# Kernel optimization log

Hardware: AMD Instinct MI355X
Metric: run time of the kernel (lower is better)

Reference implementation:

```python
import jax, jax.numpy as jnp
import numpy as np

B, T, I, H, O = 128, 1024, 512, 1024, 512
LN_EPS = 1e-5

def _linear_params(key, out_dim, in_dim):
    k1, k2 = jax.random.split(key)
    bound = 1.0 / np.sqrt(in_dim)
    W = jax.random.uniform(k1, (out_dim, in_dim), jnp.float32, -bound, bound)
    b = jax.random.uniform(k2, (out_dim,), jnp.float32, -bound, bound)
    return W, b

def setup_inputs() -> dict:
    key = jax.random.key(0)
    ks = jax.random.split(key, 10)
    x = jax.random.normal(ks[0], (B, T, I), jnp.float32)
    Wir, bir = _linear_params(ks[1], H, I)
    Whr, bhr = _linear_params(ks[2], H, H)
    Wiz, biz = _linear_params(ks[3], H, I)
    Whz, bhz = _linear_params(ks[4], H, H)
    Win, bin_ = _linear_params(ks[5], H, I)
    Whn, bhn = _linear_params(ks[6], H, H)
    Wskip, bskip = _linear_params(ks[7], H, I)
    gamma = jnp.ones((H,), jnp.float32)
    beta = jnp.zeros((H,), jnp.float32)
    Wout, bout = _linear_params(ks[8], O, H)
    return dict(x=x, Wir=Wir, bir=bir, Whr=Whr, bhr=bhr, Wiz=Wiz, biz=biz,
                Whz=Whz, bhz=bhz, Win=Win, bin_=bin_, Whn=Whn, bhn=bhn,
                Wskip=Wskip, bskip=bskip, gamma=gamma, beta=beta,
                Wout=Wout, bout=bout)

def reference(x, Wir, bir, Whr, bhr, Wiz, biz, Whz, bhz, Win, bin_, Whn, bhn,
              Wskip, bskip, gamma, beta, Wout, bout):
    # Precompute input-side projections in one batched GEMM each (same math as per-step Linear).
    rx = jnp.einsum('bti,hi->bth', x, Wir) + bir  # (B,T,H)
    zx = jnp.einsum('bti,hi->bth', x, Wiz) + biz
    nx = jnp.einsum('bti,hi->bth', x, Win) + bin_

    def step(h, inp):
        rx_t, zx_t, nx_t = inp
        r = jax.nn.sigmoid(rx_t + h @ Whr.T + bhr)
        z = jax.nn.sigmoid(zx_t + h @ Whz.T + bhz)
        n = jnp.tanh(nx_t + r * (h @ Whn.T + bhn))
        h_new = (1.0 - z) * n + z * h
        return h_new, h_new

    h0 = jnp.zeros((x.shape[0], Whr.shape[0]), x.dtype)
    xs = (jnp.swapaxes(rx, 0, 1), jnp.swapaxes(zx, 0, 1), jnp.swapaxes(nx, 0, 1))
    _, hs = jax.lax.scan(step, h0, xs)  # hs: (T,B,H)
    hs = jnp.swapaxes(hs, 0, 1)  # (B,T,H)

    skip = jnp.einsum('bti,hi->bth', x, Wskip) + bskip
    combined = hs + skip
    mu = jnp.mean(combined, axis=-1, keepdims=True)
    var = jnp.var(combined, axis=-1, keepdims=True)
    normed = (combined - mu) * jax.lax.rsqrt(var + LN_EPS) * gamma + beta
    out = jnp.einsum('bth,oh->bto', normed, Wout) + bout  # (B,T,O)
    return out
```

## Files before the change

### kernel.cpp

```cpp
#include <hip/hip_runtime.h>

#define T_DIM 1024
#define B_DIM 128
#define I_DIM 512
#define H_DIM 1024
#define O_DIM 512
#define TC 64
#define NCHUNK (T_DIM / TC)

typedef _Float16 half8 __attribute__((ext_vector_type(8)));
typedef _Float16 half4v __attribute__((ext_vector_type(4)));
typedef float floatx4 __attribute__((ext_vector_type(4)));
typedef unsigned int uint4v __attribute__((ext_vector_type(4)));

__device__ __forceinline__ void gload_lds16(const void* g, void* l) {
  __builtin_amdgcn_global_load_lds(
      (const __attribute__((address_space(1))) void*)g,
      (__attribute__((address_space(3))) void*)l, 16, 0, 0);
}

__device__ __forceinline__ float sigmoidf_(float x) {
  return 1.f / (1.f + __expf(-x));
}
__device__ __forceinline__ float tanhf_(float x) {
  float e = __expf(fminf(-2.f * x, 60.f));
  return (1.f - e) / (1.f + e);
}

__global__ __launch_bounds__(256) void k_cvt(const float* __restrict__ s,
                                             _Float16* __restrict__ d, int n4) {
  int i = blockIdx.x * 256 + threadIdx.x;
  if (i < n4) {
    float4 v = ((const float4*)s)[i];
    half4v h = {(_Float16)v.x, (_Float16)v.y, (_Float16)v.z, (_Float16)v.w};
    ((half4v*)d)[i] = h;
  }
}

__global__ __launch_bounds__(256) void k_cvt_x(const float* __restrict__ x,
                                               _Float16* __restrict__ x16, int t0) {
  int i = blockIdx.x * 256 + threadIdx.x;
  int i4 = i & 127;
  int row = i >> 7;
  int b = row & 127, tl = row >> 7;
  float4 v = ((const float4*)(x + ((size_t)b * T_DIM + t0 + tl) * I_DIM))[i4];
  half4v h = {(_Float16)v.x, (_Float16)v.y, (_Float16)v.z, (_Float16)v.w};
  ((half4v*)(x16 + (size_t)row * I_DIM))[i4] = h;
}

__global__ __launch_bounds__(256) void build_bcat(const float* __restrict__ a,
                                                  const float* __restrict__ b,
                                                  const float* __restrict__ c,
                                                  const float* __restrict__ d,
                                                  float* __restrict__ o) {
  int i = blockIdx.x * 256 + threadIdx.x;
  if (i < 4096) {
    const float* p = (i < 1024) ? a : (i < 2048) ? b : (i < 3072) ? c : d;
    o[i] = p[i & 1023];
  }
}

template <int MODE>
__global__ __launch_bounds__(256) void gemm_f16(
    const _Float16* __restrict__ A, const _Float16* __restrict__ B,
    const float* __restrict__ bias, _Float16* __restrict__ C16,
    float* __restrict__ C32, int M, int N, int K, int t0) {
  __shared__ __align__(16) _Float16 As[128 * 64];
  __shared__ __align__(16) _Float16 Bs[128 * 64];
  const int tid = threadIdx.x, lane = tid & 63, wv = tid >> 6;
  const int wm = wv >> 1, wn = wv & 1;
  const int lj = lane & 15, lk = lane >> 4;
  const size_t rowA0 = (size_t)blockIdx.y * 128, colB0 = (size_t)blockIdx.x * 128;
  floatx4 acc[4][4] = {};
  for (int kb = 0; kb < K; kb += 64) {
    __syncthreads();
#pragma unroll
    for (int i = 0; i < 4; ++i) {
      int q = i * 256 + tid;
      int r = q >> 3, c = q & 7;
      gload_lds16(A + (rowA0 + r) * (size_t)K + kb + c * 8, As + (size_t)(i * 4 + wv) * 512);
    }
#pragma unroll
    for (int i = 0; i < 4; ++i) {
      int q = i * 256 + tid;
      int r = q >> 3, c = q & 7;
      gload_lds16(B + (colB0 + r) * (size_t)K + kb + c * 8, Bs + (size_t)(i * 4 + wv) * 512);
    }
    __syncthreads();
#pragma unroll
    for (int ks = 0; ks < 2; ++ks) {
      half8 af[4], bf[4];
#pragma unroll
      for (int am = 0; am < 4; ++am)
        af[am] = *(const half8*)(As + (wm * 64 + am * 16 + lj) * 64 + ks * 32 + lk * 8);
#pragma unroll
      for (int bn = 0; bn < 4; ++bn)
        bf[bn] = *(const half8*)(Bs + (wn * 64 + bn * 16 + lj) * 64 + ks * 32 + lk * 8);
#pragma unroll
      for (int am = 0; am < 4; ++am)
#pragma unroll
        for (int bn = 0; bn < 4; ++bn)
          acc[am][bn] = __builtin_amdgcn_mfma_f32_16x16x32_f16(af[am], bf[bn], acc[am][bn], 0, 0, 0);
    }
  }
#pragma unroll
  for (int am = 0; am < 4; ++am)
#pragma unroll
    for (int bn = 0; bn < 4; ++bn)
#pragma unroll
      for (int rr = 0; rr < 4; ++rr) {
        size_t grow = rowA0 + wm * 64 + am * 16 + lk * 4 + rr;
        size_t gcol = colB0 + wn * 64 + bn * 16 + lj;
        float v = acc[am][bn][rr] + bias[gcol];
        if constexpr (MODE == 0) {
          C16[grow * (size_t)N + gcol] = (_Float16)v;
        } else {
          size_t tl = grow >> 7, b = grow & 127;
          C32[b * (size_t)(T_DIM * O_DIM) + (t0 + tl) * (size_t)O_DIM + gcol] = v;
        }
      }
}

__global__ __launch_bounds__(384) void scan_kernel(
    const _Float16* __restrict__ rznx,
    const _Float16* __restrict__ Whcat,
    const float* __restrict__ bhr, const float* __restrict__ bhz,
    const float* __restrict__ bhn,
    _Float16* __restrict__ h16,
    float* __restrict__ h32,
    _Float16* __restrict__ hs16,
    int* __restrict__ flags,
    int chunk) {
  __shared__ __align__(16) _Float16 hlds[16 * 1024];
  __shared__ float exch[2][2][16 * 17];
  __shared__ __align__(16) _Float16 hout[16][32];
  const int tid = threadIdx.x, lane = tid & 63, wv = tid >> 6;
  const int g = wv % 3, jh = wv / 3;
  const int bg = blockIdx.x & 7, js = blockIdx.x >> 3;
  const int b0 = bg * 16;
  const int jbase = js * 32 + jh * 16;
  const int lj = lane & 15, lk = lane >> 4;
  const int jcol = jbase + lj;

  half8 wf[32];
  {
    const _Float16* wb = Whcat + ((size_t)g * 1024 + jcol) * 1024 + lk * 8;
#pragma unroll
    for (int ks = 0; ks < 32; ++ks) wf[ks] = *(const half8*)(wb + ks * 32);
  }
  const float* bh = (g == 0) ? bhr : (g == 1) ? bhz : bhn;
  const float biasg = bh[jcol];
  float hown[4];
  if (g == 1) {
#pragma unroll
    for (int r = 0; r < 4; ++r) hown[r] = h32[(size_t)(b0 + lk * 4 + r) * 1024 + jcol];
  }
  int cur = 0;
  for (int t = 0; t < TC; ++t) {
    const int gs = chunk * TC + t;
    const _Float16* xg = rznx + ((size_t)t * 128 + b0) * 4096 + g * 1024 + jcol;
    float xv[4];
#pragma unroll
    for (int r = 0; r < 4; ++r) xv[r] = (float)xg[(size_t)(lk * 4 + r) * 4096];
    float nxv[4];
    if (g == 1) {
#pragma unroll
      for (int r = 0; r < 4; ++r)
        nxv[r] = (float)rznx[((size_t)t * 128 + b0 + lk * 4 + r) * 4096 + 2048 + jcol];
    }
    if (tid < 256) {
      const _Float16* hsrc = h16 + (size_t)cur * (128 * 1024) + (size_t)b0 * 1024;
      uint4v vv[8];
      const char* ap[8];
#pragma unroll
      for (int i = 0; i < 8; ++i) {
        int q = tid + i * 256;
        int b = q >> 7, c = q & 127;
        ap[i] = (const char*)(hsrc + b * 1024 + c * 8);
      }
#pragma unroll
      for (int i = 0; i < 8; ++i)
        asm volatile("global_load_dwordx4 %0, %1, off sc0 sc1"
                     : "=v"(vv[i]) : "v"(ap[i]));
      asm volatile("s_waitcnt vmcnt(0)" ::: "memory");
#pragma unroll
      for (int i = 0; i < 8; ++i) {
        int q = tid + i * 256;
        int b = q >> 7, c = q & 127;
        *(uint4v*)((char*)hlds + b * 2048 + ((c ^ (b & 7)) * 16)) = vv[i];
      }
    }
    __syncthreads();
    floatx4 acc = {0.f, 0.f, 0.f, 0.f};
#pragma unroll
    for (int ks = 0; ks < 32; ++ks) {
      int c = ks * 4 + lk;
      int b = lj;
      half8 af = *(const half8*)((const char*)hlds + b * 2048 + ((c ^ (b & 7)) * 16));
      acc = __builtin_amdgcn_mfma_f32_16x16x32_f16(af, wf[ks], acc, 0, 0, 0);
    }
    float zv[4] = {0.f, 0.f, 0.f, 0.f};
    if (g == 0) {
#pragma unroll
      for (int r = 0; r < 4; ++r)
        exch[jh][0][(lk * 4 + r) * 17 + lj] = sigmoidf_(acc[r] + biasg + xv[r]);
    } else if (g == 2) {
#pragma unroll
      for (int r = 0; r < 4; ++r)
        exch[jh][1][(lk * 4 + r) * 17 + lj] = acc[r] + biasg;
    } else {
#pragma unroll
      for (int r = 0; r < 4; ++r) zv[r] = sigmoidf_(acc[r] + biasg + xv[r]);
    }
    __syncthreads();
    if (g == 1) {
#pragma unroll
      for (int r = 0; r < 4; ++r) {
        float rr = exch[jh][0][(lk * 4 + r) * 17 + lj];
        float np = exch[jh][1][(lk * 4 + r) * 17 + lj];
        float n = tanhf_(nxv[r] + rr * np);
        float hn = (1.f - zv[r]) * n + zv[r] * hown[r];
        hown[r] = hn;
        hout[lk * 4 + r][jh * 16 + lj] = (_Float16)hn;
      }
    }
    __syncthreads();
    if (wv == 0) {
      int row = lane >> 2, c = lane & 3;
      uint4v hv = *(const uint4v*)((const char*)hout + row * 64 + c * 16);
      char* p1 = (char*)(h16 + (size_t)(cur ^ 1) * (128 * 1024) +
                         (size_t)(b0 + row) * 1024 + js * 32 + c * 8);
      asm volatile("global_store_dwordx4 %0, %1, off sc0 sc1"
                   :: "v"(p1), "v"(hv) : "memory");
      _Float16* p2 = hs16 + ((size_t)t * 128 + b0 + row) * 1024 + js * 32 + c * 8;
      *(uint4v*)p2 = hv;
      asm volatile("s_waitcnt vmcnt(0)" ::: "memory");
      if (lane == 0) {
        int* fp = flags + ((size_t)bg * 32 + js) * 32;
        int val = gs + 1;
        asm volatile("global_store_dword %0, %1, off sc0 sc1"
                     :: "v"(fp), "v"(val) : "memory");
      }
    } else if (wv == 5) {
      const int* fp = flags + ((size_t)bg * 32 + (lane & 31)) * 32;
      const int target = gs + 1;
      int spin = 0;
      while (true) {
        int v;
        asm volatile("global_load_dword %0, %1, off sc0 sc1\n\ts_waitcnt vmcnt(0)"
                     : "=v"(v) : "v"(fp) : "memory");
        if (__all(v >= target)) break;
        __builtin_amdgcn_s_sleep(1);
        if (++spin > (1 << 17)) break;
      }
    }
    __syncthreads();
    cur ^= 1;
  }
  if (g == 1) {
#pragma unroll
    for (int r = 0; r < 4; ++r) h32[(size_t)(b0 + lk * 4 + r) * 1024 + jcol] = hown[r];
  }
}

__global__ __launch_bounds__(256) void ln_kernel(
    const _Float16* __restrict__ hs, const _Float16* __restrict__ rz,
    const float* __restrict__ gamma, const float* __restrict__ beta,
    _Float16* __restrict__ outp) {
  const int row = blockIdx.x, tid = threadIdx.x;
  const int lane = tid & 63, wv = tid >> 6;
  half4v hv = *(const half4v*)(hs + (size_t)row * 1024 + tid * 4);
  half4v sv = *(const half4v*)(rz + (size_t)row * 4096 + 3072 + tid * 4);
  float v[4];
  float s = 0.f, s2 = 0.f;
#pragma unroll
  for (int j = 0; j < 4; ++j) {
    v[j] = (float)hv[j] + (float)sv[j];
    s += v[j];
    s2 += v[j] * v[j];
  }
#pragma unroll
  for (int o = 32; o > 0; o >>= 1) {
    s += __shfl_xor(s, o, 64);
    s2 += __shfl_xor(s2, o, 64);
  }
  __shared__ float ps[4][2];
  if (lane == 0) { ps[wv][0] = s; ps[wv][1] = s2; }
  __syncthreads();
  s = ps[0][0] + ps[1][0] + ps[2][0] + ps[3][0];
  s2 = ps[0][1] + ps[1][1] + ps[2][1] + ps[3][1];
  const float mu = s * (1.f / 1024.f);
  const float var = s2 * (1.f / 1024.f) - mu * mu;
  const float rstd = rsqrtf(var + 1e-5f);
  half4v ov;
#pragma unroll
  for (int j = 0; j < 4; ++j)
    ov[j] = (_Float16)((v[j] - mu) * rstd * gamma[tid * 4 + j] + beta[tid * 4 + j]);
  *(half4v*)(outp + (size_t)row * 1024 + tid * 4) = ov;
}

extern "C" void kernel_launch(void* const* d_in, const int* in_sizes, int n_in,
                              void* d_out, int out_size, void* d_ws, size_t ws_size,
                              hipStream_t stream) {
  const float* x     = (const float*)d_in[0];
  const float* Wir   = (const float*)d_in[1];
  const float* bir   = (const float*)d_in[2];
  const float* Whr   = (const float*)d_in[3];
  const float* bhr   = (const float*)d_in[4];
  const float* Wiz   = (const float*)d_in[5];
  const float* biz   = (const float*)d_in[6];
  const float* Whz   = (const float*)d_in[7];
  const float* bhz   = (const float*)d_in[8];
  const float* Win   = (const float*)d_in[9];
  const float* bin_  = (const float*)d_in[10];
  const float* Whn   = (const float*)d_in[11];
  const float* bhn   = (const float*)d_in[12];
  const float* Wskip = (const float*)d_in[13];
  const float* bskip = (const float*)d_in[14];
  const float* gamma = (const float*)d_in[15];
  const float* beta  = (const float*)d_in[16];
  const float* Wout  = (const float*)d_in[17];
  const float* bout  = (const float*)d_in[18];
  float* out = (float*)d_out;

  char* ws = (char*)d_ws;
  size_t off = 0;
  auto alloc = [&](size_t bytes) -> char* {
    char* p = ws + off;
    off += (bytes + 255) & ~(size_t)255;
    return p;
  };
  _Float16* x16    = (_Float16*)alloc((size_t)TC * 128 * 512 * 2);
  _Float16* Wcat   = (_Float16*)alloc((size_t)4096 * 512 * 2);
  _Float16* Whcat  = (_Float16*)alloc((size_t)3072 * 1024 * 2);
  _Float16* Wout16 = (_Float16*)alloc((size_t)512 * 1024 * 2);
  float*    bcat   = (float*)alloc(4096 * 4);
  _Float16* rznx   = (_Float16*)alloc((size_t)TC * 128 * 4096 * 2);
  _Float16* h16    = (_Float16*)alloc((size_t)2 * 128 * 1024 * 2);
  float*    h32    = (float*)alloc((size_t)128 * 1024 * 4);
  _Float16* hs16   = (_Float16*)alloc((size_t)TC * 128 * 1024 * 2);
  _Float16* normed = (_Float16*)alloc((size_t)TC * 128 * 1024 * 2);
  int*      flags  = (int*)alloc(8 * 32 * 32 * sizeof(int));

  k_cvt<<<512, 256, 0, stream>>>(Wir, Wcat + 0 * 524288, 131072);
  k_cvt<<<512, 256, 0, stream>>>(Wiz, Wcat + 1 * 524288, 131072);
  k_cvt<<<512, 256, 0, stream>>>(Win, Wcat + 2 * 524288, 131072);
  k_cvt<<<512, 256, 0, stream>>>(Wskip, Wcat + 3 * 524288, 131072);
  k_cvt<<<1024, 256, 0, stream>>>(Whr, Whcat + 0 * 1048576, 262144);
  k_cvt<<<1024, 256, 0, stream>>>(Whz, Whcat + 1 * 1048576, 262144);
  k_cvt<<<1024, 256, 0, stream>>>(Whn, Whcat + 2 * 1048576, 262144);
  k_cvt<<<512, 256, 0, stream>>>(Wout, Wout16, 131072);
  build_bcat<<<16, 256, 0, stream>>>(bir, biz, bin_, bskip, bcat);
  hipMemsetAsync(h16, 0, (size_t)2 * 128 * 1024 * 2, stream);
  hipMemsetAsync(h32, 0, (size_t)128 * 1024 * 4, stream);
  hipMemsetAsync(flags, 0, 8 * 32 * 32 * sizeof(int), stream);

  for (int c = 0; c < NCHUNK; ++c) {
    int t0 = c * TC;
    k_cvt_x<<<(TC * 128 * 512 / 4) / 256, 256, 0, stream>>>(x, x16, t0);
    gemm_f16<0><<<dim3(4096 / 128, TC * 128 / 128), 256, 0, stream>>>(
        x16, Wcat, bcat, rznx, nullptr, TC * 128, 4096, 512, 0);
    scan_kernel<<<256, 384, 0, stream>>>(rznx, Whcat, bhr, bhz, bhn, h16, h32, hs16, flags, c);
    ln_kernel<<<TC * 128, 256, 0, stream>>>(hs16, rznx, gamma, beta, normed);
    gemm_f16<1><<<dim3(512 / 128, TC * 128 / 128), 256, 0, stream>>>(
        normed, Wout16, bout, nullptr, out, TC * 128, 512, 1024, t0);
  }
}
```

Before: 5.329 ms.

## Replace flag-based grid barrier with step-tagged hidden state words

```diff
diff --git a/kernel.cpp b/kernel.cpp
--- a/kernel.cpp
+++ b/kernel.cpp
@@ -126,10 +126,9 @@
     const _Float16* __restrict__ Whcat,
     const float* __restrict__ bhr, const float* __restrict__ bhz,
     const float* __restrict__ bhn,
-    _Float16* __restrict__ h16,
+    unsigned* __restrict__ htag,
     float* __restrict__ h32,
     _Float16* __restrict__ hs16,
-    int* __restrict__ flags,
     int chunk) {
   __shared__ __align__(16) _Float16 hlds[16 * 1024];
   __shared__ float exch[2][2][16 * 17];
@@ -155,7 +154,14 @@
 #pragma unroll
     for (int r = 0; r < 4; ++r) hown[r] = h32[(size_t)(b0 + lk * 4 + r) * 1024 + jcol];
   }
-  int cur = 0;
+  int myb[6], myc[6];
+  int nmine = 0;
+#pragma unroll
+  for (int i = 0; i < 6; ++i) {
+    int q = tid + i * 384;
+    if (q < 2048) { myb[nmine] = q >> 7; myc[nmine] = q & 127; ++nmine; }
+  }
+
   for (int t = 0; t < TC; ++t) {
     const int gs = chunk * TC + t;
     const _Float16* xg = rznx + ((size_t)t * 128 + b0) * 4096 + g * 1024 + jcol;
@@ -168,37 +174,65 @@
       for (int r = 0; r < 4; ++r)
         nxv[r] = (float)rznx[((size_t)t * 128 + b0 + lk * 4 + r) * 4096 + 2048 + jcol];
     }
-    if (tid < 256) {
-      const _Float16* hsrc = h16 + (size_t)cur * (128 * 1024) + (size_t)b0 * 1024;
-      uint4v vv[8];
-      const char* ap[8];
-#pragma unroll
-      for (int i = 0; i < 8; ++i) {
-        int q = tid + i * 256;
-        int b = q >> 7, c = q & 127;
-        ap[i] = (const char*)(hsrc + b * 1024 + c * 8);
-      }
-#pragma unroll
-      for (int i = 0; i < 8; ++i)
-        asm volatile("global_load_dwordx4 %0, %1, off sc0 sc1"
-                     : "=v"(vv[i]) : "v"(ap[i]));
+    {
+      const unsigned want = (unsigned)(gs & 0xffff);
+      const unsigned* hsrc = htag + (size_t)(gs & 1) * (128 * 1024) + (size_t)b0 * 1024;
+      uint4v va[6], vb[6];
+      const char* ap[6];
+#pragma unroll
+      for (int i = 0; i < 6; ++i) {
+        if (i < nmine) {
+          ap[i] = (const char*)(hsrc + myb[i] * 1024 + myc[i] * 8);
+          asm volatile("global_load_dwordx4 %0, %1, off sc0 sc1" : "=v"(va[i]) : "v"(ap[i]));
+          asm volatile("global_load_dwordx4 %0, %1, off offset:16 sc0 sc1" : "=v"(vb[i]) : "v"(ap[i]));
+        }
+      }
       asm volatile("s_waitcnt vmcnt(0)" ::: "memory");
-#pragma unroll
-      for (int i = 0; i < 8; ++i) {
-        int q = tid + i * 256;
-        int b = q >> 7, c = q & 127;
-        *(uint4v*)((char*)hlds + b * 2048 + ((c ^ (b & 7)) * 16)) = vv[i];
-      }
-    }
-    __syncthreads();
-    floatx4 acc = {0.f, 0.f, 0.f, 0.f};
-#pragma unroll
-    for (int ks = 0; ks < 32; ++ks) {
-      int c = ks * 4 + lk;
+      int spin = 0;
+      while (true) {
+        bool okall = true;
+#pragma unroll
+        for (int i = 0; i < 6; ++i) {
+          if (i < nmine) {
+            unsigned bad = ((va[i].x >> 16) ^ want) | ((va[i].y >> 16) ^ want) |
+                           ((va[i].z >> 16) ^ want) | ((va[i].w >> 16) ^ want) |
+                           ((vb[i].x >> 16) ^ want) | ((vb[i].y >> 16) ^ want) |
+                           ((vb[i].z >> 16) ^ want) | ((vb[i].w >> 16) ^ want);
+            if (bad) {
+              okall = false;
+              asm volatile("global_load_dwordx4 %0, %1, off sc0 sc1" : "=v"(va[i]) : "v"(ap[i]));
+              asm volatile("global_load_dwordx4 %0, %1, off offset:16 sc0 sc1" : "=v"(vb[i]) : "v"(ap[i]));
+            }
+          }
+        }
+        if (okall) break;
+        asm volatile("s_waitcnt vmcnt(0)" ::: "memory");
+        if (++spin > (1 << 17)) break;
+      }
+#pragma unroll
+      for (int i = 0; i < 6; ++i) {
+        if (i < nmine) {
+          uint4v p;
+          p.x = (va[i].x & 0xffffu) | (va[i].y << 16);
+          p.y = (va[i].z & 0xffffu) | (va[i].w << 16);
+          p.z = (vb[i].x & 0xffffu) | (vb[i].y << 16);
+          p.w = (vb[i].z & 0xffffu) | (vb[i].w << 16);
+          *(uint4v*)((char*)hlds + myb[i] * 2048 + ((myc[i] ^ (myb[i] & 7)) * 16)) = p;
+        }
+      }
+    }
+    __syncthreads();
+    floatx4 acc0 = {0.f, 0.f, 0.f, 0.f}, acc1 = {0.f, 0.f, 0.f, 0.f};
+#pragma unroll
+    for (int ks = 0; ks < 32; ks += 2) {
+      int c0 = ks * 4 + lk, c1 = (ks + 1) * 4 + lk;
       int b = lj;
-      half8 af = *(const half8*)((const char*)hlds + b * 2048 + ((c ^ (b & 7)) * 16));
-      acc = __builtin_amdgcn_mfma_f32_16x16x32_f16(af, wf[ks], acc, 0, 0, 0);
-    }
+      half8 af0 = *(const half8*)((const char*)hlds + b * 2048 + ((c0 ^ (b & 7)) * 16));
+      half8 af1 = *(const half8*)((const char*)hlds + b * 2048 + ((c1 ^ (b & 7)) * 16));
+      acc0 = __builtin_amdgcn_mfma_f32_16x16x32_f16(af0, wf[ks], acc0, 0, 0, 0);
+      acc1 = __builtin_amdgcn_mfma_f32_16x16x32_f16(af1, wf[ks + 1], acc1, 0, 0, 0);
+    }
+    floatx4 acc = acc0 + acc1;
     float zv[4] = {0.f, 0.f, 0.f, 0.f};
     if (g == 0) {
 #pragma unroll
@@ -226,36 +260,21 @@
     }
     __syncthreads();
     if (wv == 0) {
-      int row = lane >> 2, c = lane & 3;
-      uint4v hv = *(const uint4v*)((const char*)hout + row * 64 + c * 16);
-      char* p1 = (char*)(h16 + (size_t)(cur ^ 1) * (128 * 1024) +
-                         (size_t)(b0 + row) * 1024 + js * 32 + c * 8);
-      asm volatile("global_store_dwordx4 %0, %1, off sc0 sc1"
-                   :: "v"(p1), "v"(hv) : "memory");
-      _Float16* p2 = hs16 + ((size_t)t * 128 + b0 + row) * 1024 + js * 32 + c * 8;
+      const unsigned ntag = (unsigned)((gs + 1) & 0xffff) << 16;
+      int row = lane >> 2, sub = lane & 3;
+      uint4v hv = *(const uint4v*)((const char*)hout + row * 64 + sub * 16);
+      unsigned* dst = htag + (size_t)((gs + 1) & 1) * (128 * 1024) +
+                      (size_t)(b0 + row) * 1024 + js * 32 + sub * 8;
+      uint4v ta, tb;
+      ta.x = ntag | (hv.x & 0xffffu);  ta.y = ntag | (hv.x >> 16);
+      ta.z = ntag | (hv.y & 0xffffu);  ta.w = ntag | (hv.y >> 16);
+      tb.x = ntag | (hv.z & 0xffffu);  tb.y = ntag | (hv.z >> 16);
+      tb.z = ntag | (hv.w & 0xffffu);  tb.w = ntag | (hv.w >> 16);
+      asm volatile("global_store_dwordx4 %0, %1, off sc0 sc1" :: "v"(dst), "v"(ta) : "memory");
+      asm volatile("global_store_dwordx4 %0, %1, off offset:16 sc0 sc1" :: "v"(dst), "v"(tb) : "memory");
+      _Float16* p2 = hs16 + ((size_t)t * 128 + b0 + row) * 1024 + js * 32 + sub * 8;
       *(uint4v*)p2 = hv;
-      asm volatile("s_waitcnt vmcnt(0)" ::: "memory");
-      if (lane == 0) {
-        int* fp = flags + ((size_t)bg * 32 + js) * 32;
-        int val = gs + 1;
-        asm volatile("global_store_dword %0, %1, off sc0 sc1"
-                     :: "v"(fp), "v"(val) : "memory");
-      }
-    } else if (wv == 5) {
-      const int* fp = flags + ((size_t)bg * 32 + (lane & 31)) * 32;
-      const int target = gs + 1;
-      int spin = 0;
-      while (true) {
-        int v;
-        asm volatile("global_load_dword %0, %1, off sc0 sc1\n\ts_waitcnt vmcnt(0)"
-                     : "=v"(v) : "v"(fp) : "memory");
-        if (__all(v >= target)) break;
-        __builtin_amdgcn_s_sleep(1);
-        if (++spin > (1 << 17)) break;
-      }
-    }
-    __syncthreads();
-    cur ^= 1;
+    }
   }
   if (g == 1) {
 #pragma unroll
@@ -336,11 +355,10 @@
   _Float16* Wout16 = (_Float16*)alloc((size_t)512 * 1024 * 2);
   float*    bcat   = (float*)alloc(4096 * 4);
   _Float16* rznx   = (_Float16*)alloc((size_t)TC * 128 * 4096 * 2);
-  _Float16* h16    = (_Float16*)alloc((size_t)2 * 128 * 1024 * 2);
+  unsigned* htag   = (unsigned*)alloc((size_t)2 * 128 * 1024 * 4);
   float*    h32    = (float*)alloc((size_t)128 * 1024 * 4);
   _Float16* hs16   = (_Float16*)alloc((size_t)TC * 128 * 1024 * 2);
   _Float16* normed = (_Float16*)alloc((size_t)TC * 128 * 1024 * 2);
-  int*      flags  = (int*)alloc(8 * 32 * 32 * sizeof(int));
 
   k_cvt<<<512, 256, 0, stream>>>(Wir, Wcat + 0 * 524288, 131072);
   k_cvt<<<512, 256, 0, stream>>>(Wiz, Wcat + 1 * 524288, 131072);
@@ -351,16 +369,15 @@
   k_cvt<<<1024, 256, 0, stream>>>(Whn, Whcat + 2 * 1048576, 262144);
   k_cvt<<<512, 256, 0, stream>>>(Wout, Wout16, 131072);
   build_bcat<<<16, 256, 0, stream>>>(bir, biz, bin_, bskip, bcat);
-  hipMemsetAsync(h16, 0, (size_t)2 * 128 * 1024 * 2, stream);
+  hipMemsetAsync(htag, 0, (size_t)2 * 128 * 1024 * 4, stream);
   hipMemsetAsync(h32, 0, (size_t)128 * 1024 * 4, stream);
-  hipMemsetAsync(flags, 0, 8 * 32 * 32 * sizeof(int), stream);
 
   for (int c = 0; c < NCHUNK; ++c) {
     int t0 = c * TC;
     k_cvt_x<<<(TC * 128 * 512 / 4) / 256, 256, 0, stream>>>(x, x16, t0);
     gemm_f16<0><<<dim3(4096 / 128, TC * 128 / 128), 256, 0, stream>>>(
         x16, Wcat, bcat, rznx, nullptr, TC * 128, 4096, 512, 0);
-    scan_kernel<<<256, 384, 0, stream>>>(rznx, Whcat, bhr, bhz, bhn, h16, h32, hs16, flags, c);
+    scan_kernel<<<256, 384, 0, stream>>>(rznx, Whcat, bhr, bhz, bhn, htag, h32, hs16, c);
     ln_kernel<<<TC * 128, 256, 0, stream>>>(hs16, rznx, gamma, beta, normed);
     gemm_f16<1><<<dim3(512 / 128, TC * 128 / 128), 256, 0, stream>>>(
         normed, Wout16, bout, nullptr, out, TC * 128, 512, 1024, t0);
```

After: 7.755 ms. 45.5% more time.

## Restructure GRU scan sync to per-producer flags and compact hidden-state exchange

Applied to the files above, without the earlier changes.

```diff
diff --git a/kernel.cpp b/kernel.cpp
--- a/kernel.cpp
+++ b/kernel.cpp
@@ -35,17 +35,6 @@
     half4v h = {(_Float16)v.x, (_Float16)v.y, (_Float16)v.z, (_Float16)v.w};
     ((half4v*)d)[i] = h;
   }
-}
-
-__global__ __launch_bounds__(256) void k_cvt_x(const float* __restrict__ x,
-                                               _Float16* __restrict__ x16, int t0) {
-  int i = blockIdx.x * 256 + threadIdx.x;
-  int i4 = i & 127;
-  int row = i >> 7;
-  int b = row & 127, tl = row >> 7;
-  float4 v = ((const float4*)(x + ((size_t)b * T_DIM + t0 + tl) * I_DIM))[i4];
-  half4v h = {(_Float16)v.x, (_Float16)v.y, (_Float16)v.z, (_Float16)v.w};
-  ((half4v*)(x16 + (size_t)row * I_DIM))[i4] = h;
 }
 
 __global__ __launch_bounds__(256) void build_bcat(const float* __restrict__ a,
@@ -60,17 +49,80 @@
   }
 }
 
-template <int MODE>
-__global__ __launch_bounds__(256) void gemm_f16(
-    const _Float16* __restrict__ A, const _Float16* __restrict__ B,
-    const float* __restrict__ bias, _Float16* __restrict__ C16,
-    float* __restrict__ C32, int M, int N, int K, int t0) {
+__global__ __launch_bounds__(256) void gemm_in(
+    const float* __restrict__ x, const _Float16* __restrict__ Wcat,
+    const float* __restrict__ bias, _Float16* __restrict__ C16, int t0) {
   __shared__ __align__(16) _Float16 As[128 * 64];
   __shared__ __align__(16) _Float16 Bs[128 * 64];
   const int tid = threadIdx.x, lane = tid & 63, wv = tid >> 6;
   const int wm = wv >> 1, wn = wv & 1;
   const int lj = lane & 15, lk = lane >> 4;
   const size_t rowA0 = (size_t)blockIdx.y * 128, colB0 = (size_t)blockIdx.x * 128;
+  const int K = 512, N = 4096;
+  floatx4 acc[4][4] = {};
+  for (int kb = 0; kb < K; kb += 64) {
+    __syncthreads();
+    float4 av[8];
+#pragma unroll
+    for (int i = 0; i < 8; ++i) {
+      int u = i * 256 + tid;
+      int r = u >> 4, f4 = u & 15;
+      size_t grow = rowA0 + r;
+      size_t b = grow & 127, tl = grow >> 7;
+      av[i] = *(const float4*)(x + (b * T_DIM + t0 + tl) * I_DIM + kb + f4 * 4);
+    }
+#pragma unroll
+    for (int i = 0; i < 4; ++i) {
+      int q = i * 256 + tid;
+      int r = q >> 3, c = q & 7;
+      gload_lds16(Wcat + (colB0 + r) * (size_t)K + kb + c * 8, Bs + (size_t)(i * 4 + wv) * 512);
+    }
+#pragma unroll
+    for (int i = 0; i < 8; ++i) {
+      int u = i * 256 + tid;
+      int r = u >> 4, f4 = u & 15;
+      half4v h = {(_Float16)av[i].x, (_Float16)av[i].y, (_Float16)av[i].z, (_Float16)av[i].w};
+      *(half4v*)(As + r * 64 + f4 * 4) = h;
+    }
+    __syncthreads();
+#pragma unroll
+    for (int ks = 0; ks < 2; ++ks) {
+      half8 af[4], bf[4];
+#pragma unroll
+      for (int am = 0; am < 4; ++am)
+        af[am] = *(const half8*)(As + (wm * 64 + am * 16 + lj) * 64 + ks * 32 + lk * 8);
+#pragma unroll
+      for (int bn = 0; bn < 4; ++bn)
+        bf[bn] = *(const half8*)(Bs + (wn * 64 + bn * 16 + lj) * 64 + ks * 32 + lk * 8);
+#pragma unroll
+      for (int am = 0; am < 4; ++am)
+#pragma unroll
+        for (int bn = 0; bn < 4; ++bn)
+          acc[am][bn] = __builtin_amdgcn_mfma_f32_16x16x32_f16(af[am], bf[bn], acc[am][bn], 0, 0, 0);
+    }
+  }
+#pragma unroll
+  for (int am = 0; am < 4; ++am)
+#pragma unroll
+    for (int bn = 0; bn < 4; ++bn)
+#pragma unroll
+      for (int rr = 0; rr < 4; ++rr) {
+        size_t grow = rowA0 + wm * 64 + am * 16 + lk * 4 + rr;
+        size_t gcol = colB0 + wn * 64 + bn * 16 + lj;
+        C16[grow * (size_t)N + gcol] = (_Float16)(acc[am][bn][rr] + bias[gcol]);
+      }
+}
+
+__global__ __launch_bounds__(256) void gemm_out(
+    const _Float16* __restrict__ A, const _Float16* __restrict__ B,
+    const float* __restrict__ bias, float* __restrict__ C32, int t0) {
+  __shared__ __align__(16) _Float16 As[128 * 64];
+  __shared__ __align__(16) _Float16 Bs[128 * 64];
+  const int tid = threadIdx.x, lane = tid & 63, wv = tid >> 6;
+  const int wm = wv >> 1, wn = wv & 1;
+  const int lj = lane & 15, lk = lane >> 4;
+  const size_t rowA0 = (size_t)blockIdx.y * 128, colB0 = (size_t)blockIdx.x * 128;
+  const int K = 1024;
   floatx4 acc[4][4] = {};
   for (int kb = 0; kb < K; kb += 64) {
     __syncthreads();
@@ -111,13 +163,9 @@
       for (int rr = 0; rr < 4; ++rr) {
         size_t grow = rowA0 + wm * 64 + am * 16 + lk * 4 + rr;
         size_t gcol = colB0 + wn * 64 + bn * 16 + lj;
-        float v = acc[am][bn][rr] + bias[gcol];
-        if constexpr (MODE == 0) {
-          C16[grow * (size_t)N + gcol] = (_Float16)v;
-        } else {
-          size_t tl = grow >> 7, b = grow & 127;
-          C32[b * (size_t)(T_DIM * O_DIM) + (t0 + tl) * (size_t)O_DIM + gcol] = v;
-        }
+        size_t tl = grow >> 7, b = grow & 127;
+        C32[b * (size_t)(T_DIM * O_DIM) + (t0 + tl) * (size_t)O_DIM + gcol] =
+            acc[am][bn][rr] + bias[gcol];
       }
 }
 
@@ -126,8 +174,7 @@
     const _Float16* __restrict__ Whcat,
     const float* __restrict__ bhr, const float* __restrict__ bhz,
     const float* __restrict__ bhn,
-    _Float16* __restrict__ h16,
-    float* __restrict__ h32,
+    _Float16* __restrict__ hpub,
     _Float16* __restrict__ hs16,
     int* __restrict__ flags,
     int chunk) {
@@ -151,11 +198,11 @@
   const float* bh = (g == 0) ? bhr : (g == 1) ? bhz : bhn;
   const float biasg = bh[jcol];
   float hown[4];
-  if (g == 1) {
-#pragma unroll
-    for (int r = 0; r < 4; ++r) hown[r] = h32[(size_t)(b0 + lk * 4 + r) * 1024 + jcol];
-  }
-  int cur = 0;
+
+  const int p = tid >> 3;
+  const int i0 = tid & 7;
+  const int m0 = i0 * 8;
+
   for (int t = 0; t < TC; ++t) {
     const int gs = chunk * TC + t;
     const _Float16* xg = rznx + ((size_t)t * 128 + b0) * 4096 + g * 1024 + jcol;
@@ -169,36 +216,54 @@
         nxv[r] = (float)rznx[((size_t)t * 128 + b0 + lk * 4 + r) * 4096 + 2048 + jcol];
     }
     if (tid < 256) {
-      const _Float16* hsrc = h16 + (size_t)cur * (128 * 1024) + (size_t)b0 * 1024;
+      const int* fp = flags + ((size_t)bg * 32 + p) * 32;
+      int fv, spin = 0;
+      while (true) {
+        asm volatile("global_load_dword %0, %1, off sc0 sc1\n\ts_waitcnt vmcnt(0)"
+                     : "=v"(fv) : "v"(fp) : "memory");
+        if (fv >= gs) break;
+        if (++spin > (1 << 17)) break;
+      }
+      const char* src = (const char*)(hpub +
+          ((((size_t)(gs & 1) * 8 + bg) * 32 + p) * 512) + (size_t)m0 * 8);
       uint4v vv[8];
-      const char* ap[8];
-#pragma unroll
-      for (int i = 0; i < 8; ++i) {
-        int q = tid + i * 256;
-        int b = q >> 7, c = q & 127;
-        ap[i] = (const char*)(hsrc + b * 1024 + c * 8);
-      }
-#pragma unroll
-      for (int i = 0; i < 8; ++i)
-        asm volatile("global_load_dwordx4 %0, %1, off sc0 sc1"
-                     : "=v"(vv[i]) : "v"(ap[i]));
+      asm volatile("global_load_dwordx4 %0, %1, off sc0 sc1" : "=v"(vv[0]) : "v"(src));
+      asm volatile("global_load_dwordx4 %0, %1, off offset:16 sc0 sc1" : "=v"(vv[1]) : "v"(src));
+      asm volatile("global_load_dwordx4 %0, %1, off offset:32 sc0 sc1" : "=v"(vv[2]) : "v"(src));
+      asm volatile("global_load_dwordx4 %0, %1, off offset:48 sc0 sc1" : "=v"(vv[3]) : "v"(src));
+      asm volatile("global_load_dwordx4 %0, %1, off offset:64 sc0 sc1" : "=v"(vv[4]) : "v"(src));
+      asm volatile("global_load_dwordx4 %0, %1, off offset:80 sc0 sc1" : "=v"(vv[5]) : "v"(src));
+      asm volatile("global_load_dwordx4 %0, %1, off offset:96 sc0 sc1" : "=v"(vv[6]) : "v"(src));
+      asm volatile("global_load_dwordx4 %0, %1, off offset:112 sc0 sc1" : "=v"(vv[7]) : "v"(src));
       asm volatile("s_waitcnt vmcnt(0)" ::: "memory");
 #pragma unroll
-      for (int i = 0; i < 8; ++i) {
-        int q = tid + i * 256;
-        int b = q >> 7, c = q & 127;
-        *(uint4v*)((char*)hlds + b * 2048 + ((c ^ (b & 7)) * 16)) = vv[i];
-      }
-    }
-    __syncthreads();
-    floatx4 acc = {0.f, 0.f, 0.f, 0.f};
-#pragma unroll
-    for (int ks = 0; ks < 32; ++ks) {
-      int c = ks * 4 + lk;
+      for (int k = 0; k < 8; ++k) {
+        int m = m0 + k;
+        int row = m >> 2, cgl = m & 3;
+        int c = p * 4 + cgl;
+        *(uint4v*)((char*)hlds + row * 2048 + ((c ^ (row & 7)) * 16)) = vv[k];
+      }
+    }
+    __syncthreads();
+    if (t == 0 && g == 1) {
+#pragma unroll
+      for (int r = 0; r < 4; ++r) {
+        int b = lk * 4 + r, c = jcol >> 3;
+        hown[r] = (float)*(const _Float16*)((const char*)hlds + b * 2048 +
+                      ((c ^ (b & 7)) * 16) + (jcol & 7) * 2);
+      }
+    }
+    floatx4 acc0 = {0.f, 0.f, 0.f, 0.f}, acc1 = {0.f, 0.f, 0.f, 0.f};
+#pragma unroll
+    for (int ks = 0; ks < 32; ks += 2) {
+      int c0 = ks * 4 + lk, c1 = (ks + 1) * 4 + lk;
       int b = lj;
-      half8 af = *(const half8*)((const char*)hlds + b * 2048 + ((c ^ (b & 7)) * 16));
-      acc = __builtin_amdgcn_mfma_f32_16x16x32_f16(af, wf[ks], acc, 0, 0, 0);
-    }
+      half8 af0 = *(const half8*)((const char*)hlds + b * 2048 + ((c0 ^ (b & 7)) * 16));
+      half8 af1 = *(const half8*)((const char*)hlds + b * 2048 + ((c1 ^ (b & 7)) * 16));
+      acc0 = __builtin_amdgcn_mfma_f32_16x16x32_f16(af0, wf[ks], acc0, 0, 0, 0);
+      acc1 = __builtin_amdgcn_mfma_f32_16x16x32_f16(af1, wf[ks + 1], acc1, 0, 0, 0);
+    }
+    floatx4 acc = acc0 + acc1;
     float zv[4] = {0.f, 0.f, 0.f, 0.f};
     if (g == 0) {
 #pragma unroll
@@ -226,40 +291,20 @@
     }
     __syncthreads();
     if (wv == 0) {
-      int row = lane >> 2, c = lane & 3;
-      uint4v hv = *(const uint4v*)((const char*)hout + row * 64 + c * 16);
-      char* p1 = (char*)(h16 + (size_t)(cur ^ 1) * (128 * 1024) +
-                         (size_t)(b0 + row) * 1024 + js * 32 + c * 8);
-      asm volatile("global_store_dwordx4 %0, %1, off sc0 sc1"
-                   :: "v"(p1), "v"(hv) : "memory");
-      _Float16* p2 = hs16 + ((size_t)t * 128 + b0 + row) * 1024 + js * 32 + c * 8;
-      *(uint4v*)p2 = hv;
+      int row = lane >> 2, cgl = lane & 3;
+      uint4v hv = *(const uint4v*)((const char*)hout + row * 64 + cgl * 16);
+      char* dst = (char*)(hpub +
+          ((((size_t)((gs + 1) & 1) * 8 + bg) * 32 + js) * 512)) + (size_t)lane * 16;
+      asm volatile("global_store_dwordx4 %0, %1, off sc0 sc1" :: "v"(dst), "v"(hv) : "memory");
       asm volatile("s_waitcnt vmcnt(0)" ::: "memory");
       if (lane == 0) {
-        int* fp = flags + ((size_t)bg * 32 + js) * 32;
+        int* fpw = flags + ((size_t)bg * 32 + js) * 32;
         int val = gs + 1;
-        asm volatile("global_store_dword %0, %1, off sc0 sc1"
-                     :: "v"(fp), "v"(val) : "memory");
-      }
-    } else if (wv == 5) {
-      const int* fp = flags + ((size_t)bg * 32 + (lane & 31)) * 32;
-      const int target = gs + 1;
-      int spin = 0;
-      while (true) {
-        int v;
-        asm volatile("global_load_dword %0, %1, off sc0 sc1\n\ts_waitcnt vmcnt(0)"
-                     : "=v"(v) : "v"(fp) : "memory");
-        if (__all(v >= target)) break;
-        __builtin_amdgcn_s_sleep(1);
-        if (++spin > (1 << 17)) break;
-      }
-    }
-    __syncthreads();
-    cur ^= 1;
-  }
-  if (g == 1) {
-#pragma unroll
-    for (int r = 0; r < 4; ++r) h32[(size_t)(b0 + lk * 4 + r) * 1024 + jcol] = hown[r];
+        asm volatile("global_store_dword %0, %1, off sc0 sc1" :: "v"(fpw), "v"(val) : "memory");
+      }
+      _Float16* p2 = hs16 + ((size_t)t * 128 + b0 + row) * 1024 + js * 32 + cgl * 8;
+      *(uint4v*)p2 = hv;
+    }
   }
 }
 
@@ -330,14 +375,12 @@
     off += (bytes + 255) & ~(size_t)255;
     return p;
   };
-  _Float16* x16    = (_Float16*)alloc((size_t)TC * 128 * 512 * 2);
   _Float16* Wcat   = (_Float16*)alloc((size_t)4096 * 512 * 2);
   _Float16* Whcat  = (_Float16*)alloc((size_t)3072 * 1024 * 2);
   _Float16* Wout16 = (_Float16*)alloc((size_t)512 * 1024 * 2);
   float*    bcat   = (float*)alloc(4096 * 4);
   _Float16* rznx   = (_Float16*)alloc((size_t)TC * 128 * 4096 * 2);
-  _Float16* h16    = (_Float16*)alloc((size_t)2 * 128 * 1024 * 2);
-  float*    h32    = (float*)alloc((size_t)128 * 1024 * 4);
+  _Float16* hpub   = (_Float16*)alloc((size_t)2 * 8 * 32 * 512 * 2);
   _Float16* hs16   = (_Float16*)alloc((size_t)TC * 128 * 1024 * 2);
   _Float16* normed = (_Float16*)alloc((size_t)TC * 128 * 1024 * 2);
   int*      flags  = (int*)alloc(8 * 32 * 32 * sizeof(int));
@@ -351,18 +394,14 @@
   k_cvt<<<1024, 256, 0, stream>>>(Whn, Whcat + 2 * 1048576, 262144);
   k_cvt<<<512, 256, 0, stream>>>(Wout, Wout16, 131072);
   build_bcat<<<16, 256, 0, stream>>>(bir, biz, bin_, bskip, bcat);
-  hipMemsetAsync(h16, 0, (size_t)2 * 128 * 1024 * 2, stream);
-  hipMemsetAsync(h32, 0, (size_t)128 * 1024 * 4, stream);
+  hipMemsetAsync(hpub, 0, (size_t)2 * 8 * 32 * 512 * 2, stream);
   hipMemsetAsync(flags, 0, 8 * 32 * 32 * sizeof(int), stream);
 
   for (int c = 0; c < NCHUNK; ++c) {
     int t0 = c * TC;
-    k_cvt_x<<<(TC * 128 * 512 / 4) / 256, 256, 0, stream>>>(x, x16, t0);
-    gemm_f16<0><<<dim3(4096 / 128, TC * 128 / 128), 256, 0, stream>>>(
-        x16, Wcat, bcat, rznx, nullptr, TC * 128, 4096, 512, 0);
-    scan_kernel<<<256, 384, 0, stream>>>(rznx, Whcat, bhr, bhz, bhn, h16, h32, hs16, flags, c);
+    gemm_in<<<dim3(32, 64), 256, 0, stream>>>(x, Wcat, bcat, rznx, t0);
+    scan_kernel<<<256, 384, 0, stream>>>(rznx, Whcat, bhr, bhz, bhn, hpub, hs16, flags, c);
     ln_kernel<<<TC * 128, 256, 0, stream>>>(hs16, rznx, gamma, beta, normed);
-    gemm_f16<1><<<dim3(512 / 128, TC * 128 / 128), 256, 0, stream>>>(
-        normed, Wout16, bout, nullptr, out, TC * 128, 512, 1024, t0);
-  }
-}
+    gemm_out<<<dim3(4, 64), 256, 0, stream>>>(normed, Wout16, bout, out, t0);
+  }
+}
```

Result: slower. 6.833 ms (+28.2%).

## Restructure GRU scan step: transposed MFMA, direct gate publish, per-wave flags

Applied to the files above, without the earlier changes.

```diff
diff --git a/kernel.cpp b/kernel.cpp
--- a/kernel.cpp
+++ b/kernel.cpp
@@ -12,6 +12,7 @@
 typedef _Float16 half4v __attribute__((ext_vector_type(4)));
 typedef float floatx4 __attribute__((ext_vector_type(4)));
 typedef unsigned int uint4v __attribute__((ext_vector_type(4)));
+typedef unsigned int uint2v __attribute__((ext_vector_type(2)));
 
 __device__ __forceinline__ void gload_lds16(const void* g, void* l) {
   __builtin_amdgcn_global_load_lds(
@@ -121,128 +122,122 @@
       }
 }
 
-__global__ __launch_bounds__(384) void scan_kernel(
+__global__ __launch_bounds__(384, 1) void scan_kernel(
     const _Float16* __restrict__ rznx,
     const _Float16* __restrict__ Whcat,
     const float* __restrict__ bhr, const float* __restrict__ bhz,
     const float* __restrict__ bhn,
-    _Float16* __restrict__ h16,
+    _Float16* __restrict__ hpub,
     float* __restrict__ h32,
     _Float16* __restrict__ hs16,
     int* __restrict__ flags,
     int chunk) {
   __shared__ __align__(16) _Float16 hlds[16 * 1024];
-  __shared__ float exch[2][2][16 * 17];
-  __shared__ __align__(16) _Float16 hout[16][32];
+  __shared__ __align__(16) float exch_r[2][64][4];
+  __shared__ __align__(16) float exch_n[2][64][4];
   const int tid = threadIdx.x, lane = tid & 63, wv = tid >> 6;
   const int g = wv % 3, jh = wv / 3;
   const int bg = blockIdx.x & 7, js = blockIdx.x >> 3;
   const int b0 = bg * 16;
-  const int jbase = js * 32 + jh * 16;
   const int lj = lane & 15, lk = lane >> 4;
-  const int jcol = jbase + lj;
+  const int jrow = js * 32 + jh * 16 + lj;
+  const int jcol0 = js * 32 + jh * 16 + lk * 4;
+  const int bidx = b0 + lj;
 
   half8 wf[32];
   {
-    const _Float16* wb = Whcat + ((size_t)g * 1024 + jcol) * 1024 + lk * 8;
+    const _Float16* wb = Whcat + ((size_t)g * 1024 + jrow) * 1024 + lk * 8;
 #pragma unroll
     for (int ks = 0; ks < 32; ++ks) wf[ks] = *(const half8*)(wb + ks * 32);
   }
   const float* bh = (g == 0) ? bhr : (g == 1) ? bhz : bhn;
-  const float biasg = bh[jcol];
-  float hown[4];
-  if (g == 1) {
-#pragma unroll
-    for (int r = 0; r < 4; ++r) hown[r] = h32[(size_t)(b0 + lk * 4 + r) * 1024 + jcol];
-  }
-  int cur = 0;
+  const floatx4 bias4 = *(const floatx4*)(bh + jcol0);
+  floatx4 hown;
+  if (g == 1) hown = *(const floatx4*)(h32 + (size_t)bidx * 1024 + jcol0);
+
+  const int p = tid >> 3, i0 = tid & 7;
+
   for (int t = 0; t < TC; ++t) {
     const int gs = chunk * TC + t;
-    const _Float16* xg = rznx + ((size_t)t * 128 + b0) * 4096 + g * 1024 + jcol;
-    float xv[4];
-#pragma unroll
-    for (int r = 0; r < 4; ++r) xv[r] = (float)xg[(size_t)(lk * 4 + r) * 4096];
-    float nxv[4];
+    float xv[4], nxv[4];
+    if (g == 0) {
+      half4v xh = *(const half4v*)(rznx + ((size_t)t * 128 + bidx) * 4096 + jcol0);
+#pragma unroll
+      for (int r = 0; r < 4; ++r) xv[r] = (float)xh[r];
+    } else if (g == 1) {
+      half4v xh = *(const half4v*)(rznx + ((size_t)t * 128 + bidx) * 4096 + 1024 + jcol0);
+      half4v nh = *(const half4v*)(rznx + ((size_t)t * 128 + bidx) * 4096 + 2048 + jcol0);
+#pragma unroll
+      for (int r = 0; r < 4; ++r) { xv[r] = (float)xh[r]; nxv[r] = (float)nh[r]; }
+    }
+    if (tid < 256) {
+      const char* src = (const char*)hpub +
+          ((((size_t)(gs & 1) * 8 + bg) * 32 + p) << 10) + (size_t)i0 * 128;
+      uint4v vv[8];
+      asm volatile("global_load_dwordx4 %0, %1, off sc0 sc1" : "=v"(vv[0]) : "v"(src));
+      asm volatile("global_load_dwordx4 %0, %1, off offset:16 sc0 sc1" : "=v"(vv[1]) : "v"(src));
+      asm volatile("global_load_dwordx4 %0, %1, off offset:32 sc0 sc1" : "=v"(vv[2]) : "v"(src));
+      asm volatile("global_load_dwordx4 %0, %1, off offset:48 sc0 sc1" : "=v"(vv[3]) : "v"(src));
+      asm volatile("global_load_dwordx4 %0, %1, off offset:64 sc0 sc1" : "=v"(vv[4]) : "v"(src));
+      asm volatile("global_load_dwordx4 %0, %1, off offset:80 sc0 sc1" : "=v"(vv[5]) : "v"(src));
+      asm volatile("global_load_dwordx4 %0, %1, off offset:96 sc0 sc1" : "=v"(vv[6]) : "v"(src));
+      asm volatile("global_load_dwordx4 %0, %1, off offset:112 sc0 sc1" : "=v"(vv[7]) : "v"(src));
+      asm volatile("s_waitcnt vmcnt(0)" ::: "memory");
+#pragma unroll
+      for (int k = 0; k < 8; ++k) {
+        int row = i0 * 2 + (k >> 2);
+        int c = p * 4 + (k & 3);
+        *(uint4v*)((char*)hlds + row * 2048 + ((c ^ (row & 7)) * 16)) = vv[k];
+      }
+    }
+    __syncthreads();
+    floatx4 acc0 = {0.f, 0.f, 0.f, 0.f}, acc1 = {0.f, 0.f, 0.f, 0.f};
+#pragma unroll
+    for (int ks = 0; ks < 32; ks += 2) {
+      int c0 = ks * 4 + lk, c1 = (ks + 1) * 4 + lk;
+      half8 af0 = *(const half8*)((const char*)hlds + lj * 2048 + ((c0 ^ (lj & 7)) * 16));
+      half8 af1 = *(const half8*)((const char*)hlds + lj * 2048 + ((c1 ^ (lj & 7)) * 16));
+      acc0 = __builtin_amdgcn_mfma_f32_16x16x32_f16(wf[ks], af0, acc0, 0, 0, 0);
+      acc1 = __builtin_amdgcn_mfma_f32_16x16x32_f16(wf[ks + 1], af1, acc1, 0, 0, 0);
+    }
+    floatx4 acc = acc0 + acc1;
+    floatx4 zv;
+    if (g == 0) {
+      floatx4 rv;
+#pragma unroll
+      for (int r = 0; r < 4; ++r) rv[r] = sigmoidf_(acc[r] + bias4[r] + xv[r]);
+      *(floatx4*)exch_r[jh][lane] = rv;
+    } else if (g == 2) {
+      *(floatx4*)exch_n[jh][lane] = acc + bias4;
+    } else {
+#pragma unroll
+      for (int r = 0; r < 4; ++r) zv[r] = sigmoidf_(acc[r] + bias4[r] + xv[r]);
+    }
+    __syncthreads();
     if (g == 1) {
-#pragma unroll
-      for (int r = 0; r < 4; ++r)
-        nxv[r] = (float)rznx[((size_t)t * 128 + b0 + lk * 4 + r) * 4096 + 2048 + jcol];
-    }
-    if (tid < 256) {
-      const _Float16* hsrc = h16 + (size_t)cur * (128 * 1024) + (size_t)b0 * 1024;
-      uint4v vv[8];
-      const char* ap[8];
-#pragma unroll
-      for (int i = 0; i < 8; ++i) {
-        int q = tid + i * 256;
-        int b = q >> 7, c = q & 127;
-        ap[i] = (const char*)(hsrc + b * 1024 + c * 8);
-      }
-#pragma unroll
-      for (int i = 0; i < 8; ++i)
-        asm volatile("global_load_dwordx4 %0, %1, off sc0 sc1"
-                     : "=v"(vv[i]) : "v"(ap[i]));
-      asm volatile("s_waitcnt vmcnt(0)" ::: "memory");
-#pragma unroll
-      for (int i = 0; i < 8; ++i) {
-        int q = tid + i * 256;
-        int b = q >> 7, c = q & 127;
-        *(uint4v*)((char*)hlds + b * 2048 + ((c ^ (b & 7)) * 16)) = vv[i];
-      }
-    }
-    __syncthreads();
-    floatx4 acc = {0.f, 0.f, 0.f, 0.f};
-#pragma unroll
-    for (int ks = 0; ks < 32; ++ks) {
-      int c = ks * 4 + lk;
-      int b = lj;
-      half8 af = *(const half8*)((const char*)hlds + b * 2048 + ((c ^ (b & 7)) * 16));
-      acc = __builtin_amdgcn_mfma_f32_16x16x32_f16(af, wf[ks], acc, 0, 0, 0);
-    }
-    float zv[4] = {0.f, 0.f, 0.f, 0.f};
-    if (g == 0) {
-#pragma unroll
-      for (int r = 0; r < 4; ++r)
-        exch[jh][0][(lk * 4 + r) * 17 + lj] = sigmoidf_(acc[r] + biasg + xv[r]);
-    } else if (g == 2) {
-#pragma unroll
-      for (int r = 0; r < 4; ++r)
-        exch[jh][1][(lk * 4 + r) * 17 + lj] = acc[r] + biasg;
-    } else {
-#pragma unroll
-      for (int r = 0; r < 4; ++r) zv[r] = sigmoidf_(acc[r] + biasg + xv[r]);
-    }
-    __syncthreads();
-    if (g == 1) {
+      floatx4 rv = *(const floatx4*)exch_r[jh][lane];
+      floatx4 np = *(const floatx4*)exch_n[jh][lane];
+      half4v hp;
 #pragma unroll
       for (int r = 0; r < 4; ++r) {
-        float rr = exch[jh][0][(lk * 4 + r) * 17 + lj];
-        float np = exch[jh][1][(lk * 4 + r) * 17 + lj];
-        float n = tanhf_(nxv[r] + rr * np);
+        float n = tanhf_(nxv[r] + rv[r] * np[r]);
         float hn = (1.f - zv[r]) * n + zv[r] * hown[r];
         hown[r] = hn;
-        hout[lk * 4 + r][jh * 16 + lj] = (_Float16)hn;
-      }
-    }
-    __syncthreads();
-    if (wv == 0) {
-      int row = lane >> 2, c = lane & 3;
-      uint4v hv = *(const uint4v*)((const char*)hout + row * 64 + c * 16);
-      char* p1 = (char*)(h16 + (size_t)(cur ^ 1) * (128 * 1024) +
-                         (size_t)(b0 + row) * 1024 + js * 32 + c * 8);
-      asm volatile("global_store_dwordx4 %0, %1, off sc0 sc1"
-                   :: "v"(p1), "v"(hv) : "memory");
-      _Float16* p2 = hs16 + ((size_t)t * 128 + b0 + row) * 1024 + js * 32 + c * 8;
-      *(uint4v*)p2 = hv;
+        hp[r] = (_Float16)hn;
+      }
+      uint2v u = *(uint2v*)&hp;
+      char* dst = (char*)hpub + ((((size_t)((gs + 1) & 1) * 8 + bg) * 32 + js) << 10) +
+                  (size_t)lj * 64 + jh * 32 + lk * 8;
+      asm volatile("global_store_dwordx2 %0, %1, off sc0 sc1" :: "v"(dst), "v"(u) : "memory");
+      *(uint2v*)(hs16 + ((size_t)t * 128 + bidx) * 1024 + jcol0) = u;
       asm volatile("s_waitcnt vmcnt(0)" ::: "memory");
       if (lane == 0) {
-        int* fp = flags + ((size_t)bg * 32 + js) * 32;
+        int* fpw = flags + ((size_t)bg * 64 + js * 2 + jh) * 32;
         int val = gs + 1;
-        asm volatile("global_store_dword %0, %1, off sc0 sc1"
-                     :: "v"(fp), "v"(val) : "memory");
-      }
-    } else if (wv == 5) {
-      const int* fp = flags + ((size_t)bg * 32 + (lane & 31)) * 32;
+        asm volatile("global_store_dword %0, %1, off sc0 sc1" :: "v"(fpw), "v"(val) : "memory");
+      }
+    } else if (wv == 0) {
+      const int* fp = flags + ((size_t)bg * 64 + lane) * 32;
       const int target = gs + 1;
       int spin = 0;
       while (true) {
@@ -255,12 +250,8 @@
       }
     }
     __syncthreads();
-    cur ^= 1;
-  }
-  if (g == 1) {
-#pragma unroll
-    for (int r = 0; r < 4; ++r) h32[(size_t)(b0 + lk * 4 + r) * 1024 + jcol] = hown[r];
-  }
+  }
+  if (g == 1) *(floatx4*)(h32 + (size_t)bidx * 1024 + jcol0) = hown;
 }
 
 __global__ __launch_bounds__(256) void ln_kernel(
@@ -336,11 +327,11 @@
   _Float16* Wout16 = (_Float16*)alloc((size_t)512 * 1024 * 2);
   float*    bcat   = (float*)alloc(4096 * 4);
   _Float16* rznx   = (_Float16*)alloc((size_t)TC * 128 * 4096 * 2);
-  _Float16* h16    = (_Float16*)alloc((size_t)2 * 128 * 1024 * 2);
+  _Float16* hpub   = (_Float16*)alloc((size_t)2 * 8 * 32 * 512 * 2);
   float*    h32    = (float*)alloc((size_t)128 * 1024 * 4);
   _Float16* hs16   = (_Float16*)alloc((size_t)TC * 128 * 1024 * 2);
   _Float16* normed = (_Float16*)alloc((size_t)TC * 128 * 1024 * 2);
-  int*      flags  = (int*)alloc(8 * 32 * 32 * sizeof(int));
+  int*      flags  = (int*)alloc(8 * 64 * 32 * sizeof(int));
 
   k_cvt<<<512, 256, 0, stream>>>(Wir, Wcat + 0 * 524288, 131072);
   k_cvt<<<512, 256, 0, stream>>>(Wiz, Wcat + 1 * 524288, 131072);
@@ -351,16 +342,16 @@
   k_cvt<<<1024, 256, 0, stream>>>(Whn, Whcat + 2 * 1048576, 262144);
   k_cvt<<<512, 256, 0, stream>>>(Wout, Wout16, 131072);
   build_bcat<<<16, 256, 0, stream>>>(bir, biz, bin_, bskip, bcat);
-  hipMemsetAsync(h16, 0, (size_t)2 * 128 * 1024 * 2, stream);
+  hipMemsetAsync(hpub, 0, (size_t)2 * 8 * 32 * 512 * 2, stream);
   hipMemsetAsync(h32, 0, (size_t)128 * 1024 * 4, stream);
-  hipMemsetAsync(flags, 0, 8 * 32 * 32 * sizeof(int), stream);
+  hipMemsetAsync(flags, 0, 8 * 64 * 32 * sizeof(int), stream);
 
   for (int c = 0; c < NCHUNK; ++c) {
     int t0 = c * TC;
     k_cvt_x<<<(TC * 128 * 512 / 4) / 256, 256, 0, stream>>>(x, x16, t0);
     gemm_f16<0><<<dim3(4096 / 128, TC * 128 / 128), 256, 0, stream>>>(
         x16, Wcat, bcat, rznx, nullptr, TC * 128, 4096, 512, 0);
-    scan_kernel<<<256, 384, 0, stream>>>(rznx, Whcat, bhr, bhz, bhn, h16, h32, hs16, flags, c);
+    scan_kernel<<<256, 384, 0, stream>>>(rznx, Whcat, bhr, bhz, bhn, hpub, h32, hs16, flags, c);
     ln_kernel<<<TC * 128, 256, 0, stream>>>(hs16, rznx, gamma, beta, normed);
     gemm_f16<1><<<dim3(512 / 128, TC * 128 / 128), 256, 0, stream>>>(
         normed, Wout16, bout, nullptr, out, TC * 128, 512, 1024, t0);
```

Measured after the change: 7.220 ms. +35.5%, slower.
